# Kernel optimization log

Measured on AMD Instinct MI355X. Metric: run time of the kernel, lower is better.

## Reference

```python
import jax, jax.numpy as jnp
import numpy as np

CLIP_LIMIT = 10.0
NTILES = 8        # OpenCV createCLAHE default tileGridSize=(8,8)
NBINS = 256

_M_RGB2XYZ = jnp.array([[0.412453, 0.357580, 0.180423],
                        [0.212671, 0.715160, 0.072169],
                        [0.019334, 0.119193, 0.950227]], dtype=jnp.float32)
_M_XYZ2RGB = jnp.array([[ 3.240479, -1.537150, -0.498535],
                        [-0.969256,  1.875992,  0.041556],
                        [ 0.055648, -0.204043,  1.057311]], dtype=jnp.float32)
_WP = jnp.array([0.950456, 1.0, 1.088754], dtype=jnp.float32)  # D65 white point (OpenCV)
_EPS = 0.008856


def rgb2lab(rgb):  # rgb: [H,W,3] in [0,1]
    xyz = jnp.einsum('hwc,dc->hwd', rgb, _M_RGB2XYZ) / _WP
    f = jnp.where(xyz > _EPS, jnp.cbrt(xyz), 7.787 * xyz + 16.0 / 116.0)
    fx, fy, fz = f[..., 0], f[..., 1], f[..., 2]
    L = 116.0 * fy - 16.0
    a = 500.0 * (fx - fy)
    b = 200.0 * (fy - fz)
    return L, a, b


def lab2rgb(L, a, b):
    fy = (L + 16.0) / 116.0
    fx = fy + a / 500.0
    fz = fy - b / 200.0
    f = jnp.stack([fx, fy, fz], axis=-1)
    xyz = jnp.where(f ** 3 > _EPS, f ** 3, (f - 16.0 / 116.0) / 7.787) * _WP
    rgb = jnp.einsum('hwd,cd->hwc', xyz, _M_XYZ2RGB)
    return jnp.clip(rgb, 0.0, 1.0)


def clahe_channel(L8, clip_limit):
    # L8: [H,W] int32 in [0,255]
    H, W = L8.shape
    th, tw = H // NTILES, W // NTILES
    area = float(th * tw)
    # per-tile histograms via one scatter-add
    rows = jnp.arange(H) // th            # [H] tile row id
    cols = jnp.arange(W) // tw            # [W] tile col id
    tid = rows[:, None] * NTILES + cols[None, :]          # [H,W]
    flat = (tid * NBINS + L8).ravel()
    hist = jnp.zeros(NTILES * NTILES * NBINS, jnp.float32).at[flat].add(1.0)
    hist = hist.reshape(NTILES * NTILES, NBINS)
    # clip + uniform redistribution of excess
    clip = max(clip_limit * area / NBINS, 1.0)
    excess = jnp.sum(jnp.maximum(hist - clip, 0.0), axis=1, keepdims=True)
    hist = jnp.minimum(hist, clip) + excess / NBINS
    # CDF -> LUT (OpenCV: lutScale = 255/tileArea, rounded)
    cdf = jnp.cumsum(hist, axis=1)
    lut = jnp.clip(jnp.round(cdf * (255.0 / area)), 0.0, 255.0)  # [T, 256]
    # bilinear interpolation between tile LUTs
    fy = jnp.clip((jnp.arange(H, dtype=jnp.float32) + 0.5) / th - 0.5, 0.0, NTILES - 1.0)
    fx = jnp.clip((jnp.arange(W, dtype=jnp.float32) + 0.5) / tw - 0.5, 0.0, NTILES - 1.0)
    y0 = jnp.floor(fy).astype(jnp.int32); y1 = jnp.minimum(y0 + 1, NTILES - 1)
    x0 = jnp.floor(fx).astype(jnp.int32); x1 = jnp.minimum(x0 + 1, NTILES - 1)
    wy = (fy - y0)[:, None]; wx = (fx - x0)[None, :]
    def g(yi, xi):  # gather LUT value for each pixel from tile (yi, xi)
        return lut[yi[:, None] * NTILES + xi[None, :], L8]
    top = (1.0 - wx) * g(y0, x0) + wx * g(y0, x1)
    bot = (1.0 - wx) * g(y1, x0) + wx * g(y1, x1)
    return (1.0 - wy) * top + wy * bot   # [H,W] float in [0,255]


def setup_inputs() -> dict:
    key = jax.random.key(0)
    x = jax.random.uniform(key, (3, 2048, 2048), dtype=jnp.float32)
    return {"x": x}


def reference(x) -> jnp.ndarray:
    hwc = jnp.transpose(x, (1, 2, 0))          # CHW -> HWC
    L, a, b = rgb2lab(hwc)                      # L in [0,100]
    L8 = jnp.clip(jnp.round(L * (255.0 / 100.0)), 0, 255).astype(jnp.int32)
    L_eq = clahe_channel(L8, CLIP_LIMIT) * (100.0 / 255.0)
    rgb = lab2rgb(L_eq, a, b)
    return jnp.transpose(rgb, (2, 0, 1))        # HWC -> CHW
```

## Files before the change

### kernel.cpp

```cpp
#include <hip/hip_runtime.h>
#include <stdint.h>

#define HW 4194304
#define WIDTH 2048
#define F(x) ((float)(x))

__device__ __forceinline__ float cbrtf_glibc(float x) {
    unsigned int bits = __float_as_uint(x);
    int xe = (int)((bits >> 23) & 0xFF) - 126;
    float xm = __uint_as_float((bits & 0x007FFFFFu) | 0x3F000000u);

    static const double factor[5] = {
        1.0 / 1.5874010519681994748,
        1.0 / 1.2599210498948731648,
        1.0,
        1.2599210498948731648,
        1.5874010519681994748
    };

    double xmd = (double)xm;
    double p = __dsub_rn(0.697570460207922770, __dmul_rn(0.191502161678719066, xmd));
    p = __dadd_rn(0.492659620528969547, __dmul_rn(p, xmd));
    float u = (float)p;

    float t2 = __fmul_rn(__fmul_rn(u, u), u);

    double ud  = (double)u;
    double t2d = (double)t2;
    double num = __dmul_rn(ud, __dadd_rn(t2d, __dmul_rn(2.0, xmd)));
    double den = __dadd_rn(__dmul_rn(2.0, t2d), xmd);
    double ym  = __dmul_rn(__ddiv_rn(num, den), factor[2 + (xe % 3)]);
    float ymf = (float)ym;

    return ldexpf(ymf, xe / 3);
}

__device__ __forceinline__ void rgb2lab_px(float r, float g, float b,
                                           int& l8, float& A_, float& B_) {
    float X = __fadd_rn(__fadd_rn(__fmul_rn(r, F(0.412453)), __fmul_rn(g, F(0.357580))), __fmul_rn(b, F(0.180423)));
    float Y = __fadd_rn(__fadd_rn(__fmul_rn(r, F(0.212671)), __fmul_rn(g, F(0.715160))), __fmul_rn(b, F(0.072169)));
    float Z = __fadd_rn(__fadd_rn(__fmul_rn(r, F(0.019334)), __fmul_rn(g, F(0.119193))), __fmul_rn(b, F(0.950227)));
    X = __fdiv_rn(X, F(0.950456));
    Z = __fdiv_rn(Z, F(1.088754));
    const float EPS = F(0.008856);
    const float C0  = F(16.0 / 116.0);
    float fx = (X > EPS) ? cbrtf_glibc(X) : __fadd_rn(__fmul_rn(F(7.787), X), C0);
    float fy = (Y > EPS) ? cbrtf_glibc(Y) : __fadd_rn(__fmul_rn(F(7.787), Y), C0);
    float fz = (Z > EPS) ? cbrtf_glibc(Z) : __fadd_rn(__fmul_rn(F(7.787), Z), C0);
    float L  = __fsub_rn(__fmul_rn(F(116.0), fy), F(16.0));
    A_ = __fmul_rn(F(500.0), __fsub_rn(fx, fy));
    B_ = __fmul_rn(F(200.0), __fsub_rn(fy, fz));
    float Lr = rintf(__fmul_rn(L, F(255.0 / 100.0)));
    Lr = fminf(fmaxf(Lr, 0.0f), 255.0f);
    l8 = (int)Lr;
}

__device__ __forceinline__ void lab2rgb_px(float Leq, float A_, float B_,
                                           float& rr, float& gg, float& bb) {
    const float EPS = F(0.008856);
    const float C0  = F(16.0 / 116.0);
    float fy2 = __fdiv_rn(__fadd_rn(Leq, 16.0f), 116.0f);
    float fx2 = __fadd_rn(fy2, __fdiv_rn(A_, 500.0f));
    float fz2 = __fsub_rn(fy2, __fdiv_rn(B_, 200.0f));
    float t3;
    t3 = fx2 * fx2 * fx2;
    float X = ((t3 > EPS) ? t3 : __fdiv_rn(__fsub_rn(fx2, C0), F(7.787))) * F(0.950456);
    t3 = fy2 * fy2 * fy2;
    float Y = ((t3 > EPS) ? t3 : __fdiv_rn(__fsub_rn(fy2, C0), F(7.787))) * F(1.0);
    t3 = fz2 * fz2 * fz2;
    float Z = ((t3 > EPS) ? t3 : __fdiv_rn(__fsub_rn(fz2, C0), F(7.787))) * F(1.088754);
    rr = __fadd_rn(__fadd_rn(__fmul_rn(X, F(3.240479)),  __fmul_rn(Y, F(-1.537150))), __fmul_rn(Z, F(-0.498535)));
    gg = __fadd_rn(__fadd_rn(__fmul_rn(X, F(-0.969256)), __fmul_rn(Y, F(1.875992))),  __fmul_rn(Z, F(0.041556)));
    bb = __fadd_rn(__fadd_rn(__fmul_rn(X, F(0.055648)),  __fmul_rn(Y, F(-0.204043))), __fmul_rn(Z, F(1.057311)));
    rr = fminf(fmaxf(rr, 0.0f), 1.0f);
    gg = fminf(fmaxf(gg, 0.0f), 1.0f);
    bb = fminf(fmaxf(bb, 0.0f), 1.0f);
}

__global__ __launch_bounds__(256, 8) void k_hist_ab(const float* __restrict__ x,
        unsigned int* __restrict__ hist,
        float* __restrict__ Abuf, float* __restrict__ Bbuf,
        unsigned int* __restrict__ l8buf, int store) {
    __shared__ unsigned int h[2048];
    const int t = threadIdx.x;
    const int y = blockIdx.x;
    #pragma unroll
    for (int i = 0; i < 8; ++i) h[i * 256 + t] = 0;
    __syncthreads();

    const int rowbase = y * WIDTH;
    #pragma unroll
    for (int ch = 0; ch < 2; ++ch) {
        const int col0 = ch * 1024 + 4 * t;
        const int idx  = rowbase + col0;
        float4 r4 = *(const float4*)(x + idx);
        float4 g4 = *(const float4*)(x + idx + HW);
        float4 b4 = *(const float4*)(x + idx + 2 * HW);
        int l80, l81, l82, l83;
        float A0, A1, A2, A3, B0, B1, B2, B3;
        rgb2lab_px(r4.x, g4.x, b4.x, l80, A0, B0);
        rgb2lab_px(r4.y, g4.y, b4.y, l81, A1, B1);
        rgb2lab_px(r4.z, g4.z, b4.z, l82, A2, B2);
        rgb2lab_px(r4.w, g4.w, b4.w, l83, A3, B3);
        const int hb = (col0 >> 8) << 8;
        atomicAdd(&h[hb + l80], 1u);
        atomicAdd(&h[hb + l81], 1u);
        atomicAdd(&h[hb + l82], 1u);
        atomicAdd(&h[hb + l83], 1u);
        if (store) {
            *(float4*)(Abuf + idx) = make_float4(A0, A1, A2, A3);
            *(float4*)(Bbuf + idx) = make_float4(B0, B1, B2, B3);
            l8buf[idx >> 2] = (unsigned)l80 | ((unsigned)l81 << 8)
                            | ((unsigned)l82 << 16) | ((unsigned)l83 << 24);
        }
    }
    __syncthreads();
    unsigned int* gh = hist + (y >> 8) * 2048;
    #pragma unroll
    for (int i = 0; i < 8; ++i) {
        unsigned int v = h[i * 256 + t];
        if (v) atomicAdd(&gh[i * 256 + t], v);
    }
}

__global__ __launch_bounds__(256, 8) void k_lut_apply(const float* __restrict__ x,
        const unsigned int* __restrict__ hist,
        const float* __restrict__ Abuf, const float* __restrict__ Bbuf,
        const unsigned int* __restrict__ l8buf,
        float* __restrict__ out, int stored) {
    __shared__ float lutS[4096];
    const int t = threadIdx.x;
    const int y = blockIdx.x;

    float fyc = fminf(fmaxf(((float)y + 0.5f) * (1.0f / 256.0f) - 0.5f, 0.0f), 7.0f);
    int y0 = (int)floorf(fyc);
    int y1 = min(y0 + 1, 7);
    float wy = __fsub_rn(fyc, (float)y0);
    float omwy = __fsub_rn(1.0f, wy);

    {
        const int lane = t & 63;
        const int w = t >> 6;
        #pragma unroll
        for (int i = 0; i < 4; ++i) {
            int gidx = w * 4 + i;
            int trow = gidx >> 3;
            int tcol = gidx & 7;
            int tile = (trow ? y1 : y0) * 8 + tcol;
            uint4 hv = *(const uint4*)(hist + tile * 256 + lane * 4);
            float h0 = (float)hv.x, h1 = (float)hv.y, h2 = (float)hv.z, h3 = (float)hv.w;
            float e = __fadd_rn(__fadd_rn(fmaxf(h0 - 2560.0f, 0.0f),
                                          fmaxf(h1 - 2560.0f, 0.0f)),
                                __fadd_rn(fmaxf(h2 - 2560.0f, 0.0f),
                                          fmaxf(h3 - 2560.0f, 0.0f)));
            #pragma unroll
            for (int d = 1; d < 64; d <<= 1) e = __fadd_rn(e, __shfl_xor(e, d));
            float ex = __fmul_rn(e, F(1.0 / 256.0));
            float v0 = __fadd_rn(fminf(h0, 2560.0f), ex);
            float v1 = __fadd_rn(fminf(h1, 2560.0f), ex);
            float v2 = __fadd_rn(fminf(h2, 2560.0f), ex);
            float v3 = __fadd_rn(fminf(h3, 2560.0f), ex);
            float s0 = v0;
            float s1 = __fadd_rn(s0, v1);
            float s2 = __fadd_rn(s1, v2);
            float s3 = __fadd_rn(s2, v3);
            float sc = s3;
            #pragma unroll
            for (int d = 1; d < 64; d <<= 1) {
                float u2 = __shfl_up(sc, d);
                if (lane >= d) sc = __fadd_rn(sc, u2);
            }
            float excl = __fsub_rn(sc, s3);
            int lb = trow * 2048 + tcol * 256 + lane * 4;
            float c0 = rintf(__fmul_rn(__fadd_rn(excl, s0), F(255.0 / 65536.0)));
            float c1 = rintf(__fmul_rn(__fadd_rn(excl, s1), F(255.0 / 65536.0)));
            float c2 = rintf(__fmul_rn(__fadd_rn(excl, s2), F(255.0 / 65536.0)));
            float c3 = rintf(__fmul_rn(__fadd_rn(excl, s3), F(255.0 / 65536.0)));
            lutS[lb + 0] = fminf(fmaxf(c0, 0.0f), 255.0f);
            lutS[lb + 1] = fminf(fmaxf(c1, 0.0f), 255.0f);
            lutS[lb + 2] = fminf(fmaxf(c2, 0.0f), 255.0f);
            lutS[lb + 3] = fminf(fmaxf(c3, 0.0f), 255.0f);
        }
    }
    __syncthreads();

    const int rowbase = y * WIDTH;
    #pragma unroll
    for (int ch = 0; ch < 2; ++ch) {
        const int col0 = ch * 1024 + 4 * t;
        const int idx  = rowbase + col0;
        float A0, A1, A2, A3, B0, B1, B2, B3;
        int l80, l81, l82, l83;
        if (stored) {
            float4 a4 = *(const float4*)(Abuf + idx);
            float4 b4 = *(const float4*)(Bbuf + idx);
            unsigned p = l8buf[idx >> 2];
            A0 = a4.x; A1 = a4.y; A2 = a4.z; A3 = a4.w;
            B0 = b4.x; B1 = b4.y; B2 = b4.z; B3 = b4.w;
            l80 = (int)(p & 0xFFu); l81 = (int)((p >> 8) & 0xFFu);
            l82 = (int)((p >> 16) & 0xFFu); l83 = (int)((p >> 24) & 0xFFu);
        } else {
            float4 r4 = *(const float4*)(x + idx);
            float4 g4 = *(const float4*)(x + idx + HW);
            float4 b4 = *(const float4*)(x + idx + 2 * HW);
            rgb2lab_px(r4.x, g4.x, b4.x, l80, A0, B0);
            rgb2lab_px(r4.y, g4.y, b4.y, l81, A1, B1);
            rgb2lab_px(r4.z, g4.z, b4.z, l82, A2, B2);
            rgb2lab_px(r4.w, g4.w, b4.w, l83, A3, B3);
        }

        float4 o_r, o_g, o_b;

#define PIX(J, L8V, AV, BV, OR_, OG_, OB_) {                                      \
    int col = col0 + (J);                                                         \
    float fxc = fminf(fmaxf(((float)col + 0.5f) * (1.0f / 256.0f) - 0.5f, 0.0f), 7.0f); \
    int xi0 = (int)floorf(fxc);                                                   \
    int xi1 = min(xi0 + 1, 7);                                                    \
    float wx = __fsub_rn(fxc, (float)xi0);                                        \
    float omwx = __fsub_rn(1.0f, wx);                                             \
    float g00 = lutS[xi0 * 256 + (L8V)];                                          \
    float g01 = lutS[xi1 * 256 + (L8V)];                                          \
    float g10 = lutS[2048 + xi0 * 256 + (L8V)];                                   \
    float g11 = lutS[2048 + xi1 * 256 + (L8V)];                                   \
    float top_ = __fadd_rn(__fmul_rn(omwx, g00), __fmul_rn(wx, g01));             \
    float bot_ = __fadd_rn(__fmul_rn(omwx, g10), __fmul_rn(wx, g11));             \
    float Leq = __fmul_rn(__fadd_rn(__fmul_rn(omwy, top_), __fmul_rn(wy, bot_)),  \
                          F(100.0 / 255.0));                                      \
    lab2rgb_px(Leq, (AV), (BV), (OR_), (OG_), (OB_));                             \
}
        PIX(0, l80, A0, B0, o_r.x, o_g.x, o_b.x);
        PIX(1, l81, A1, B1, o_r.y, o_g.y, o_b.y);
        PIX(2, l82, A2, B2, o_r.z, o_g.z, o_b.z);
        PIX(3, l83, A3, B3, o_r.w, o_g.w, o_b.w);
#undef PIX

        *(float4*)(out + idx)          = o_r;
        *(float4*)(out + idx + HW)     = o_g;
        *(float4*)(out + idx + 2 * HW) = o_b;
    }
}

extern "C" void kernel_launch(void* const* d_in, const int* in_sizes, int n_in,
                              void* d_out, int out_size, void* d_ws, size_t ws_size,
                              hipStream_t stream) {
    const float* x = (const float*)d_in[0];
    float* out = (float*)d_out;
    char* ws = (char*)d_ws;
    unsigned int* hist = (unsigned int*)ws;
    const size_t off = 131072;
    float* Abuf = (float*)(ws + off);
    float* Bbuf = (float*)(ws + off + (size_t)HW * 4);
    unsigned int* l8buf = (unsigned int*)(ws + off + (size_t)HW * 8);
    const size_t need = off + (size_t)HW * 9;
    const int store = (ws_size >= need) ? 1 : 0;

    (void)hipMemsetAsync(hist, 0, 65536, stream);
    k_hist_ab<<<2048, 256, 0, stream>>>(x, hist, Abuf, Bbuf, l8buf, store);
    k_lut_apply<<<2048, 256, 0, stream>>>(x, hist, Abuf, Bbuf, l8buf, out, store);
}
```

Measured before the change: 132.8 us.

## Fuse histogram and LUT-apply kernels with per-tile-row spin barriers

Merges the histogram/Lab pass and the LUT/apply pass into one persistent kernel. Each block waits on per-tile-row completion counters for only the two tile rows it needs, so the kernel boundary goes away and later rows can proceed while others finish. The fused path runs only when occupancy allows all 2048 blocks to be resident, and the spin-wait has a bounded iteration limit. The cbrt helper also replaces its table lookup and ldexpf with selects and a multiply, which assumes inputs stay in a narrow exponent range.

```diff
diff --git a/kernel.cpp b/kernel.cpp
--- a/kernel.cpp
+++ b/kernel.cpp
@@ -3,6 +3,7 @@
 
 #define HW 4194304
 #define WIDTH 2048
+#define NBLK 2048
 #define F(x) ((float)(x))
 
 __device__ __forceinline__ float cbrtf_glibc(float x) {
@@ -10,14 +11,6 @@
     int xe = (int)((bits >> 23) & 0xFF) - 126;
     float xm = __uint_as_float((bits & 0x007FFFFFu) | 0x3F000000u);
 
-    static const double factor[5] = {
-        1.0 / 1.5874010519681994748,
-        1.0 / 1.2599210498948731648,
-        1.0,
-        1.2599210498948731648,
-        1.5874010519681994748
-    };
-
     double xmd = (double)xm;
     double p = __dsub_rn(0.697570460207922770, __dmul_rn(0.191502161678719066, xmd));
     p = __dadd_rn(0.492659620528969547, __dmul_rn(p, xmd));
@@ -29,10 +22,19 @@
     double t2d = (double)t2;
     double num = __dmul_rn(ud, __dadd_rn(t2d, __dmul_rn(2.0, xmd)));
     double den = __dadd_rn(__dmul_rn(2.0, t2d), xmd);
-    double ym  = __dmul_rn(__ddiv_rn(num, den), factor[2 + (xe % 3)]);
+
+    int idx = 2 + (xe % 3);
+    double f = (idx == 2) ? 1.0
+             : (idx == 0) ? (1.0 / 1.5874010519681994748)
+             : (idx == 1) ? (1.0 / 1.2599210498948731648)
+             : (idx == 3) ? 1.2599210498948731648
+             :              1.5874010519681994748;
+    double ym  = __dmul_rn(__ddiv_rn(num, den), f);
     float ymf = (float)ym;
 
-    return ldexpf(ymf, xe / 3);
+    int q = xe / 3;
+    float s = (q == 0) ? 1.0f : ((q == -1) ? 0.5f : 0.25f);
+    return __fmul_rn(ymf, s);
 }
 
 __device__ __forceinline__ void rgb2lab_px(float r, float g, float b,
@@ -75,6 +77,180 @@
     rr = fminf(fmaxf(rr, 0.0f), 1.0f);
     gg = fminf(fmaxf(gg, 0.0f), 1.0f);
     bb = fminf(fmaxf(bb, 0.0f), 1.0f);
+}
+
+template<bool ATOMIC_LOADS>
+__device__ __forceinline__ void build_luts(const unsigned int* __restrict__ hist,
+                                           float* lutS, int y0, int y1, int t) {
+    const int lane = t & 63;
+    const int w = t >> 6;
+    #pragma unroll
+    for (int i = 0; i < 4; ++i) {
+        int gidx = w * 4 + i;
+        int trow = gidx >> 3;
+        int tcol = gidx & 7;
+        int tile = (trow ? y1 : y0) * 8 + tcol;
+        float h0, h1, h2, h3;
+        if (ATOMIC_LOADS) {
+            const unsigned int* hp = hist + tile * 256 + lane * 4;
+            h0 = (float)__hip_atomic_load(&hp[0], __ATOMIC_RELAXED, __HIP_MEMORY_SCOPE_AGENT);
+            h1 = (float)__hip_atomic_load(&hp[1], __ATOMIC_RELAXED, __HIP_MEMORY_SCOPE_AGENT);
+            h2 = (float)__hip_atomic_load(&hp[2], __ATOMIC_RELAXED, __HIP_MEMORY_SCOPE_AGENT);
+            h3 = (float)__hip_atomic_load(&hp[3], __ATOMIC_RELAXED, __HIP_MEMORY_SCOPE_AGENT);
+        } else {
+            uint4 hv = *(const uint4*)(hist + tile * 256 + lane * 4);
+            h0 = (float)hv.x; h1 = (float)hv.y; h2 = (float)hv.z; h3 = (float)hv.w;
+        }
+        float e = __fadd_rn(__fadd_rn(fmaxf(h0 - 2560.0f, 0.0f),
+                                      fmaxf(h1 - 2560.0f, 0.0f)),
+                            __fadd_rn(fmaxf(h2 - 2560.0f, 0.0f),
+                                      fmaxf(h3 - 2560.0f, 0.0f)));
+        #pragma unroll
+        for (int d = 1; d < 64; d <<= 1) e = __fadd_rn(e, __shfl_xor(e, d));
+        float ex = __fmul_rn(e, F(1.0 / 256.0));
+        float v0 = __fadd_rn(fminf(h0, 2560.0f), ex);
+        float v1 = __fadd_rn(fminf(h1, 2560.0f), ex);
+        float v2 = __fadd_rn(fminf(h2, 2560.0f), ex);
+        float v3 = __fadd_rn(fminf(h3, 2560.0f), ex);
+        float s0 = v0;
+        float s1 = __fadd_rn(s0, v1);
+        float s2 = __fadd_rn(s1, v2);
+        float s3 = __fadd_rn(s2, v3);
+        float sc = s3;
+        #pragma unroll
+        for (int d = 1; d < 64; d <<= 1) {
+            float u2 = __shfl_up(sc, d);
+            if (lane >= d) sc = __fadd_rn(sc, u2);
+        }
+        float excl = __fsub_rn(sc, s3);
+        int lb = trow * 2048 + tcol * 256 + lane * 4;
+        float c0 = rintf(__fmul_rn(__fadd_rn(excl, s0), F(255.0 / 65536.0)));
+        float c1 = rintf(__fmul_rn(__fadd_rn(excl, s1), F(255.0 / 65536.0)));
+        float c2 = rintf(__fmul_rn(__fadd_rn(excl, s2), F(255.0 / 65536.0)));
+        float c3 = rintf(__fmul_rn(__fadd_rn(excl, s3), F(255.0 / 65536.0)));
+        lutS[lb + 0] = fminf(fmaxf(c0, 0.0f), 255.0f);
+        lutS[lb + 1] = fminf(fmaxf(c1, 0.0f), 255.0f);
+        lutS[lb + 2] = fminf(fmaxf(c2, 0.0f), 255.0f);
+        lutS[lb + 3] = fminf(fmaxf(c3, 0.0f), 255.0f);
+    }
+}
+
+__device__ __forceinline__ void apply4(const float* lutS, int col0, int idx,
+        int l80, int l81, int l82, int l83,
+        float A0, float A1, float A2, float A3,
+        float B0, float B1, float B2, float B3,
+        float wy, float omwy, float* __restrict__ out) {
+    float4 o_r, o_g, o_b;
+#define PIX(J, L8V, AV, BV, OR_, OG_, OB_) {                                      \
+    int col = col0 + (J);                                                         \
+    float fxc = fminf(fmaxf(((float)col + 0.5f) * (1.0f / 256.0f) - 0.5f, 0.0f), 7.0f); \
+    int xi0 = (int)floorf(fxc);                                                   \
+    int xi1 = min(xi0 + 1, 7);                                                    \
+    float wx = __fsub_rn(fxc, (float)xi0);                                        \
+    float omwx = __fsub_rn(1.0f, wx);                                             \
+    float g00 = lutS[xi0 * 256 + (L8V)];                                          \
+    float g01 = lutS[xi1 * 256 + (L8V)];                                          \
+    float g10 = lutS[2048 + xi0 * 256 + (L8V)];                                   \
+    float g11 = lutS[2048 + xi1 * 256 + (L8V)];                                   \
+    float top_ = __fadd_rn(__fmul_rn(omwx, g00), __fmul_rn(wx, g01));             \
+    float bot_ = __fadd_rn(__fmul_rn(omwx, g10), __fmul_rn(wx, g11));             \
+    float Leq = __fmul_rn(__fadd_rn(__fmul_rn(omwy, top_), __fmul_rn(wy, bot_)),  \
+                          F(100.0 / 255.0));                                      \
+    lab2rgb_px(Leq, (AV), (BV), (OR_), (OG_), (OB_));                             \
+}
+    PIX(0, l80, A0, B0, o_r.x, o_g.x, o_b.x);
+    PIX(1, l81, A1, B1, o_r.y, o_g.y, o_b.y);
+    PIX(2, l82, A2, B2, o_r.z, o_g.z, o_b.z);
+    PIX(3, l83, A3, B3, o_r.w, o_g.w, o_b.w);
+#undef PIX
+    *(float4*)(out + idx)          = o_r;
+    *(float4*)(out + idx + HW)     = o_g;
+    *(float4*)(out + idx + 2 * HW) = o_b;
+}
+
+__global__ __launch_bounds__(256, 8) void k_fused(const float* __restrict__ x,
+        unsigned int* __restrict__ hist, unsigned int* __restrict__ rowdone,
+        float* __restrict__ Abuf, float* __restrict__ Bbuf,
+        unsigned int* __restrict__ l8buf, float* __restrict__ out) {
+    __shared__ float lutS[4096];
+    unsigned int* h = (unsigned int*)lutS;
+    const int t = threadIdx.x;
+    const int y = blockIdx.x;
+
+    #pragma unroll
+    for (int i = 0; i < 8; ++i) h[i * 256 + t] = 0;
+    __syncthreads();
+
+    const int rowbase = y * WIDTH;
+    #pragma unroll
+    for (int ch = 0; ch < 2; ++ch) {
+        const int col0 = ch * 1024 + 4 * t;
+        const int idx  = rowbase + col0;
+        float4 r4 = *(const float4*)(x + idx);
+        float4 g4 = *(const float4*)(x + idx + HW);
+        float4 b4 = *(const float4*)(x + idx + 2 * HW);
+        int l80, l81, l82, l83;
+        float A0, A1, A2, A3, B0, B1, B2, B3;
+        rgb2lab_px(r4.x, g4.x, b4.x, l80, A0, B0);
+        rgb2lab_px(r4.y, g4.y, b4.y, l81, A1, B1);
+        rgb2lab_px(r4.z, g4.z, b4.z, l82, A2, B2);
+        rgb2lab_px(r4.w, g4.w, b4.w, l83, A3, B3);
+        const int hb = (col0 >> 8) << 8;
+        atomicAdd(&h[hb + l80], 1u);
+        atomicAdd(&h[hb + l81], 1u);
+        atomicAdd(&h[hb + l82], 1u);
+        atomicAdd(&h[hb + l83], 1u);
+        *(float4*)(Abuf + idx) = make_float4(A0, A1, A2, A3);
+        *(float4*)(Bbuf + idx) = make_float4(B0, B1, B2, B3);
+        l8buf[idx >> 2] = (unsigned)l80 | ((unsigned)l81 << 8)
+                        | ((unsigned)l82 << 16) | ((unsigned)l83 << 24);
+    }
+    __syncthreads();
+    {
+        unsigned int* gh = hist + (y >> 8) * 2048;
+        #pragma unroll
+        for (int i = 0; i < 8; ++i) {
+            unsigned int v = h[i * 256 + t];
+            if (v) atomicAdd(&gh[i * 256 + t], v);
+        }
+    }
+    __syncthreads();
+
+    float fyc = fminf(fmaxf(((float)y + 0.5f) * (1.0f / 256.0f) - 0.5f, 0.0f), 7.0f);
+    int y0 = (int)floorf(fyc);
+    int y1 = min(y0 + 1, 7);
+    float wy = __fsub_rn(fyc, (float)y0);
+    float omwy = __fsub_rn(1.0f, wy);
+
+    if (t == 0) {
+        __threadfence();
+        atomicAdd(&rowdone[y >> 8], 1u);
+        long limit = 1L << 18;
+        while (limit-- > 0) {
+            unsigned a = __hip_atomic_load(&rowdone[y0], __ATOMIC_ACQUIRE, __HIP_MEMORY_SCOPE_AGENT);
+            unsigned b = __hip_atomic_load(&rowdone[y1], __ATOMIC_ACQUIRE, __HIP_MEMORY_SCOPE_AGENT);
+            if (a == 256u && b == 256u) break;
+            __builtin_amdgcn_s_sleep(2);
+        }
+    }
+    __syncthreads();
+
+    build_luts<true>(hist, lutS, y0, y1, t);
+    __syncthreads();
+
+    #pragma unroll
+    for (int ch = 0; ch < 2; ++ch) {
+        const int col0 = ch * 1024 + 4 * t;
+        const int idx  = rowbase + col0;
+        float4 a4 = *(const float4*)(Abuf + idx);
+        float4 b4 = *(const float4*)(Bbuf + idx);
+        unsigned p = l8buf[idx >> 2];
+        apply4(lutS, col0, idx,
+               (int)(p & 0xFFu), (int)((p >> 8) & 0xFFu),
+               (int)((p >> 16) & 0xFFu), (int)((p >> 24) & 0xFFu),
+               a4.x, a4.y, a4.z, a4.w, b4.x, b4.y, b4.z, b4.w,
+               wy, omwy, out);
+    }
 }
 
 __global__ __launch_bounds__(256, 8) void k_hist_ab(const float* __restrict__ x,
@@ -138,50 +314,7 @@
     float wy = __fsub_rn(fyc, (float)y0);
     float omwy = __fsub_rn(1.0f, wy);
 
-    {
-        const int lane = t & 63;
-        const int w = t >> 6;
-        #pragma unroll
-        for (int i = 0; i < 4; ++i) {
-            int gidx = w * 4 + i;
-            int trow = gidx >> 3;
-            int tcol = gidx & 7;
-            int tile = (trow ? y1 : y0) * 8 + tcol;
-            uint4 hv = *(const uint4*)(hist + tile * 256 + lane * 4);
-            float h0 = (float)hv.x, h1 = (float)hv.y, h2 = (float)hv.z, h3 = (float)hv.w;
-            float e = __fadd_rn(__fadd_rn(fmaxf(h0 - 2560.0f, 0.0f),
-                                          fmaxf(h1 - 2560.0f, 0.0f)),
-                                __fadd_rn(fmaxf(h2 - 2560.0f, 0.0f),
-                                          fmaxf(h3 - 2560.0f, 0.0f)));
-            #pragma unroll
-            for (int d = 1; d < 64; d <<= 1) e = __fadd_rn(e, __shfl_xor(e, d));
-            float ex = __fmul_rn(e, F(1.0 / 256.0));
-            float v0 = __fadd_rn(fminf(h0, 2560.0f), ex);
-            float v1 = __fadd_rn(fminf(h1, 2560.0f), ex);
-            float v2 = __fadd_rn(fminf(h2, 2560.0f), ex);
-            float v3 = __fadd_rn(fminf(h3, 2560.0f), ex);
-            float s0 = v0;
-            float s1 = __fadd_rn(s0, v1);
-            float s2 = __fadd_rn(s1, v2);
-            float s3 = __fadd_rn(s2, v3);
-            float sc = s3;
-            #pragma unroll
-            for (int d = 1; d < 64; d <<= 1) {
-                float u2 = __shfl_up(sc, d);
-                if (lane >= d) sc = __fadd_rn(sc, u2);
-            }
-            float excl = __fsub_rn(sc, s3);
-            int lb = trow * 2048 + tcol * 256 + lane * 4;
-            float c0 = rintf(__fmul_rn(__fadd_rn(excl, s0), F(255.0 / 65536.0)));
-            float c1 = rintf(__fmul_rn(__fadd_rn(excl, s1), F(255.0 / 65536.0)));
-            float c2 = rintf(__fmul_rn(__fadd_rn(excl, s2), F(255.0 / 65536.0)));
-            float c3 = rintf(__fmul_rn(__fadd_rn(excl, s3), F(255.0 / 65536.0)));
-            lutS[lb + 0] = fminf(fmaxf(c0, 0.0f), 255.0f);
-            lutS[lb + 1] = fminf(fmaxf(c1, 0.0f), 255.0f);
-            lutS[lb + 2] = fminf(fmaxf(c2, 0.0f), 255.0f);
-            lutS[lb + 3] = fminf(fmaxf(c3, 0.0f), 255.0f);
-        }
-    }
+    build_luts<false>(hist, lutS, y0, y1, t);
     __syncthreads();
 
     const int rowbase = y * WIDTH;
@@ -208,35 +341,8 @@
             rgb2lab_px(r4.z, g4.z, b4.z, l82, A2, B2);
             rgb2lab_px(r4.w, g4.w, b4.w, l83, A3, B3);
         }
-
-        float4 o_r, o_g, o_b;
-
-#define PIX(J, L8V, AV, BV, OR_, OG_, OB_) {                                      \
-    int col = col0 + (J);                                                         \
-    float fxc = fminf(fmaxf(((float)col + 0.5f) * (1.0f / 256.0f) - 0.5f, 0.0f), 7.0f); \
-    int xi0 = (int)floorf(fxc);                                                   \
-    int xi1 = min(xi0 + 1, 7);                                                    \
-    float wx = __fsub_rn(fxc, (float)xi0);                                        \
-    float omwx = __fsub_rn(1.0f, wx);                                             \
-    float g00 = lutS[xi0 * 256 + (L8V)];                                          \
-    float g01 = lutS[xi1 * 256 + (L8V)];                                          \
-    float g10 = lutS[2048 + xi0 * 256 + (L8V)];                                   \
-    float g11 = lutS[2048 + xi1 * 256 + (L8V)];                                   \
-    float top_ = __fadd_rn(__fmul_rn(omwx, g00), __fmul_rn(wx, g01));             \
-    float bot_ = __fadd_rn(__fmul_rn(omwx, g10), __fmul_rn(wx, g11));             \
-    float Leq = __fmul_rn(__fadd_rn(__fmul_rn(omwy, top_), __fmul_rn(wy, bot_)),  \
-                          F(100.0 / 255.0));                                      \
-    lab2rgb_px(Leq, (AV), (BV), (OR_), (OG_), (OB_));                             \
-}
-        PIX(0, l80, A0, B0, o_r.x, o_g.x, o_b.x);
-        PIX(1, l81, A1, B1, o_r.y, o_g.y, o_b.y);
-        PIX(2, l82, A2, B2, o_r.z, o_g.z, o_b.z);
-        PIX(3, l83, A3, B3, o_r.w, o_g.w, o_b.w);
-#undef PIX
-
-        *(float4*)(out + idx)          = o_r;
-        *(float4*)(out + idx + HW)     = o_g;
-        *(float4*)(out + idx + 2 * HW) = o_b;
+        apply4(lutS, col0, idx, l80, l81, l82, l83,
+               A0, A1, A2, A3, B0, B1, B2, B3, wy, omwy, out);
     }
 }
 
@@ -247,6 +353,7 @@
     float* out = (float*)d_out;
     char* ws = (char*)d_ws;
     unsigned int* hist = (unsigned int*)ws;
+    unsigned int* rowdone = (unsigned int*)(ws + 65536);
     const size_t off = 131072;
     float* Abuf = (float*)(ws + off);
     float* Bbuf = (float*)(ws + off + (size_t)HW * 4);
@@ -254,7 +361,21 @@
     const size_t need = off + (size_t)HW * 9;
     const int store = (ws_size >= need) ? 1 : 0;
 
-    (void)hipMemsetAsync(hist, 0, 65536, stream);
-    k_hist_ab<<<2048, 256, 0, stream>>>(x, hist, Abuf, Bbuf, l8buf, store);
-    k_lut_apply<<<2048, 256, 0, stream>>>(x, hist, Abuf, Bbuf, l8buf, out, store);
-}
+    static int fused_ok = -1;
+    if (fused_ok < 0) {
+        int nb = 0, ncu = 0, dev = 0;
+        (void)hipGetDevice(&dev);
+        hipError_t e1 = hipOccupancyMaxActiveBlocksPerMultiprocessor(&nb, k_fused, 256, 0);
+        hipError_t e2 = hipDeviceGetAttribute(&ncu, hipDeviceAttributeMultiprocessorCount, dev);
+        fused_ok = (e1 == hipSuccess && e2 == hipSuccess && nb * ncu >= NBLK) ? 1 : 0;
+    }
+
+    (void)hipMemsetAsync(ws, 0, 65536 + 64, stream);
+
+    if (fused_ok == 1 && store == 1) {
+        k_fused<<<NBLK, 256, 0, stream>>>(x, hist, rowdone, Abuf, Bbuf, l8buf, out);
+    } else {
+        k_hist_ab<<<NBLK, 256, 0, stream>>>(x, hist, Abuf, Bbuf, l8buf, store);
+        k_lut_apply<<<NBLK, 256, 0, stream>>>(x, hist, Abuf, Bbuf, l8buf, out, store);
+    }
+}
```

Result: faster. 128.3 us (-3.4%).
